# Optimization experiments

Measured on AMD Instinct MI355X. Metric: run time of the kernel, lower is better.

The kernel has to match this reference:

```python
import jax, jax.numpy as jnp
import numpy as np

B, S, DIM = 2, 2048, 2048
NH = 16
D_NOPE, D_ROPE, D_V = 128, 64, 128
D_QK = D_NOPE + D_ROPE  # 192
KV_RANK = 512
RMS_EPS = 1e-6


def setup_inputs() -> dict:
    key = jax.random.key(0)
    ks = jax.random.split(key, 8)
    x = jax.random.normal(ks[0], (B, S, DIM), dtype=jnp.float32)
    # rotary freqs as (cos, sin) pairs: [S, D_ROPE//2, 2]
    pos = jnp.arange(S, dtype=jnp.float32)
    inv_freq = 1.0 / (10000.0 ** (jnp.arange(0, D_ROPE, 2, dtype=jnp.float32) / D_ROPE))
    ang = pos[:, None] * inv_freq[None, :]
    freqs_cis = jnp.stack([jnp.cos(ang), jnp.sin(ang)], axis=-1)
    # causal mask [S, S]
    mask = jnp.where(jnp.arange(S)[None, :] > jnp.arange(S)[:, None], -jnp.inf, 0.0).astype(jnp.float32)
    sd = lambda k, shp, fan: jax.random.normal(k, shp, dtype=jnp.float32) * (fan ** -0.5)
    wq = sd(ks[1], (NH * D_QK, DIM), DIM)
    wkv_a = sd(ks[2], (KV_RANK + D_ROPE, DIM), DIM)
    wkv_b = sd(ks[3], (NH * (D_NOPE + D_V), KV_RANK), KV_RANK)
    wo = sd(ks[4], (DIM, NH * D_V), NH * D_V)
    kv_norm_w = jnp.ones((KV_RANK,), dtype=jnp.float32)
    return {"x": x, "start_pos": 0, "freqs_cis": freqs_cis, "mask": mask,
            "wq": wq, "wkv_a": wkv_a, "wkv_b": wkv_b, "wo": wo, "kv_norm_w": kv_norm_w}


def _rope(x, freqs):
    # x: [b, s, h, d] with d even; freqs: [s, d//2, 2] (cos, sin)
    b, s, h, d = x.shape
    xr = x.reshape(b, s, h, d // 2, 2)
    cos = freqs[None, :, None, :, 0]
    sin = freqs[None, :, None, :, 1]
    ye = xr[..., 0] * cos - xr[..., 1] * sin
    yo = xr[..., 0] * sin + xr[..., 1] * cos
    return jnp.stack([ye, yo], axis=-1).reshape(b, s, h, d)


def _rms_norm(x, w):
    var = jnp.mean(jnp.square(x), axis=-1, keepdims=True)
    return x * jax.lax.rsqrt(var + RMS_EPS) * w


def reference(x, start_pos, freqs_cis, mask, wq, wkv_a, wkv_b, wo, kv_norm_w):
    b, s, _ = x.shape
    scale = D_QK ** -0.5
    # query projection -> [b, s, h, d_qk]
    q = jnp.einsum('bsd,ed->bse', x, wq).reshape(b, s, NH, D_QK)
    q_nope, q_pe = q[..., :D_NOPE], q[..., D_NOPE:]
    q_pe = _rope(q_pe, freqs_cis)
    q = jnp.concatenate([q_nope, q_pe], axis=-1)
    # latent kv projection -> [b, s, kv_rank + d_rope]
    kv = jnp.einsum('bsd,ed->bse', x, wkv_a)
    kv_lat, k_pe = kv[..., :KV_RANK], kv[..., KV_RANK:]
    k_pe = _rope(k_pe[:, :, None, :], freqs_cis)  # [b, s, 1, d_rope]
    kv_up = jnp.einsum('bsr,er->bse', _rms_norm(kv_lat, kv_norm_w), wkv_b)
    kv_up = kv_up.reshape(b, s, NH, D_NOPE + D_V)
    k_nope, v = kv_up[..., :D_NOPE], kv_up[..., D_NOPE:]
    k = jnp.concatenate([k_nope, jnp.broadcast_to(k_pe, (b, s, NH, D_ROPE))], axis=-1)
    # start_pos = 0 prefill: cache[:end_pos] == freshly computed k, v
    scores = jnp.einsum('bshd,bthd->bsht', q, k) * scale
    if mask is not None:
        scores = scores + mask[None, :, None, :]
    probs = jax.nn.softmax(scores.astype(jnp.float32), axis=-1).astype(x.dtype)
    out = jnp.einsum('bsht,bthd->bshd', probs, v)
    return jnp.einsum('bse,de->bsd', out.reshape(b, s, NH * D_V), wo)
```

## Files before the change

### kernel.cpp

```cpp
#include <hip/hip_runtime.h>
#include <hip/hip_bf16.h>


typedef __bf16 bf16x8 __attribute__((ext_vector_type(8)));
typedef float  f32x4  __attribute__((ext_vector_type(4)));
typedef float  f32x16 __attribute__((ext_vector_type(16)));
typedef unsigned short us8 __attribute__((ext_vector_type(8)));
typedef unsigned short us4 __attribute__((ext_vector_type(4)));
typedef unsigned int   ui4 __attribute__((ext_vector_type(4)));

#define S_LEN   2048
#define BS_TOT  4096
#define NH      16
#define DQK     192
#define DV      128
#define KV_RANK 512
#define QSTR    3840

__device__ inline unsigned short f2bf(float f) {
  __hip_bfloat16 h = __float2bfloat16(f);
  return *reinterpret_cast<unsigned short*>(&h);
}
__device__ inline float bfu2f(unsigned short u) {
  unsigned int x = ((unsigned int)u) << 16;
  return __builtin_bit_cast(float, x);
}
__device__ inline unsigned int pack2bf(float a, float b) {
  return (unsigned int)f2bf(a) | ((unsigned int)f2bf(b) << 16);
}
__device__ inline void glds16(const void* g, void* l) {
  __builtin_amdgcn_global_load_lds(
      (const __attribute__((address_space(1))) unsigned int*)g,
      (__attribute__((address_space(3))) unsigned int*)l, 16, 0, 0);
}

__global__ __launch_bounds__(256) void cast_all_kernel(
    const float* __restrict__ x, const float* __restrict__ wq,
    const float* __restrict__ wkva, const float* __restrict__ wkvb,
    const float* __restrict__ wo,
    __hip_bfloat16* __restrict__ xb, __hip_bfloat16* __restrict__ wqb,
    __hip_bfloat16* __restrict__ wkvab, __hip_bfloat16* __restrict__ wkvbb,
    __hip_bfloat16* __restrict__ wob) {
  const int bid = blockIdx.x;
  const float* src; __hip_bfloat16* dst; int n, npad, b0, nb;
  if (bid < 771)       { src = x;    dst = xb;    n = 8388608; npad = 8388608; b0 = 0;    nb = 771; }
  else if (bid < 1349) { src = wq;   dst = wqb;   n = 6291456; npad = 6291456; b0 = 771;  nb = 578; }
  else if (bid < 1469) { src = wkva; dst = wkvab; n = 1179648; npad = 1572864; b0 = 1349; nb = 120; }
  else if (bid < 1662) { src = wkvb; dst = wkvbb; n = 2097152; npad = 2097152; b0 = 1469; nb = 193; }
  else                 { src = wo;   dst = wob;   n = 4194304; npad = 4194304; b0 = 1662; nb = 386; }
  const int tid = (bid - b0) * 256 + threadIdx.x;
  const int stride = nb * 256;
  for (int i = tid * 4; i < npad; i += stride * 4) {
    if (i + 3 < n) {
      f32x4 v = *(const f32x4*)(src + i);
      dst[i + 0] = __float2bfloat16(v.x);
      dst[i + 1] = __float2bfloat16(v.y);
      dst[i + 2] = __float2bfloat16(v.z);
      dst[i + 3] = __float2bfloat16(v.w);
    } else {
#pragma unroll
      for (int z = 0; z < 4; z++)
        dst[i + z] = __float2bfloat16((i + z < n) ? src[i + z] : 0.f);
    }
  }
}

template<int OUT_BF16>
__global__ __launch_bounds__(512, 2) void gemm_bt256(
    const __hip_bfloat16* __restrict__ A, const __hip_bfloat16* __restrict__ Bw,
    void* __restrict__ Cp, int M, int N, int K, int nbx) {
  __shared__ alignas(16) unsigned short Asl[2][256 * 64];
  __shared__ alignas(16) unsigned short Bsl[2][256 * 64];

  const int nwg = gridDim.x;
  const int cpx = nwg >> 3;
  const int id  = (blockIdx.x & 7) * cpx + (blockIdx.x >> 3);
  const int bx = id % nbx, by = id / nbx;
  const int m0 = by * 256, n0 = bx * 256;

  const int tid = threadIdx.x, w = tid >> 6, lane = tid & 63;
  const int wr = w >> 2, wc = w & 3;
  const int ml = lane & 15, quad = lane >> 4;
  const int srow = w * 8 + (lane >> 3);
  const int scol = ((lane & 7) ^ (lane >> 3)) * 8;

  const unsigned short* Ag = (const unsigned short*)A + (size_t)(m0 + srow) * K + scol;
  const unsigned short* Bg = (const unsigned short*)Bw + (size_t)(n0 + srow) * K + scol;

  f32x4 acc[8][4];
#pragma unroll
  for (int i = 0; i < 8; i++)
#pragma unroll
    for (int j = 0; j < 4; j++)
#pragma unroll
      for (int e = 0; e < 4; e++) acc[i][j][e] = 0.0f;

  auto stage = [&](int slot, int k0) {
#pragma unroll
    for (int j = 0; j < 4; j++)
      glds16(Ag + (size_t)j * 64 * K + k0, &Asl[slot][(j * 64 + w * 8) * 64]);
#pragma unroll
    for (int j = 0; j < 4; j++)
      glds16(Bg + (size_t)j * 64 * K + k0, &Bsl[slot][(j * 64 + w * 8) * 64]);
  };

  const int nt = K / 64;
  stage(0, 0);
  stage(1, 64);
  asm volatile("s_waitcnt vmcnt(8)" ::: "memory");
  __builtin_amdgcn_s_barrier();
  asm volatile("" ::: "memory");

  int slot = 0;
  for (int t = 0; t < nt; ++t) {
    const unsigned short* As = &Asl[slot][0];
    const unsigned short* Bs = &Bsl[slot][0];

    bf16x8 bfr[2][2][2];
#pragma unroll
    for (int nh = 0; nh < 2; nh++)
#pragma unroll
      for (int nf = 0; nf < 2; nf++) {
        int r = wc * 64 + nh * 32 + nf * 16 + ml;
        const char* rowp = (const char*)&Bs[r * 64];
#pragma unroll
        for (int ks = 0; ks < 2; ks++)
          bfr[nh][nf][ks] =
              *(const bf16x8*)(rowp + ((ks * 64 + quad * 16) ^ ((ml & 7) << 4)));
      }
#pragma unroll
    for (int mh = 0; mh < 2; mh++) {
      bf16x8 af[4][2];
#pragma unroll
      for (int mf = 0; mf < 4; mf++) {
        int r = wr * 128 + mh * 64 + mf * 16 + ml;
        const char* rowp = (const char*)&As[r * 64];
#pragma unroll
        for (int ks = 0; ks < 2; ks++)
          af[mf][ks] =
              *(const bf16x8*)(rowp + ((ks * 64 + quad * 16) ^ ((ml & 7) << 4)));
      }
      __builtin_amdgcn_s_setprio(1);
#pragma unroll
      for (int nh = 0; nh < 2; nh++)
#pragma unroll
        for (int mf = 0; mf < 4; mf++)
#pragma unroll
          for (int nf = 0; nf < 2; nf++)
#pragma unroll
            for (int ks = 0; ks < 2; ks++)
              acc[mh * 4 + mf][nh * 2 + nf] = __builtin_amdgcn_mfma_f32_16x16x32_bf16(
                  af[mf][ks], bfr[nh][nf][ks], acc[mh * 4 + mf][nh * 2 + nf], 0, 0, 0);
      __builtin_amdgcn_s_setprio(0);
    }

    asm volatile("" ::: "memory");
    __builtin_amdgcn_s_barrier();
    asm volatile("" ::: "memory");
    if (t + 2 < nt) {
      stage(slot, (t + 2) * 64);
      asm volatile("s_waitcnt vmcnt(8)" ::: "memory");
    } else {
      asm volatile("s_waitcnt vmcnt(0)" ::: "memory");
    }
    __builtin_amdgcn_s_barrier();
    asm volatile("" ::: "memory");
    slot ^= 1;
  }

#pragma unroll
  for (int mi = 0; mi < 8; mi++) {
#pragma unroll
    for (int ni = 0; ni < 4; ni++) {
      int col = n0 + wc * 64 + ni * 16 + ml;
      int rowb = m0 + wr * 128 + mi * 16 + quad * 4;
#pragma unroll
      for (int j = 0; j < 4; j++) {
        float v = acc[mi][ni][j];
        if (OUT_BF16)
          ((__hip_bfloat16*)Cp)[(size_t)(rowb + j) * N + col] = __float2bfloat16(v);
        else
          ((float*)Cp)[(size_t)(rowb + j) * N + col] = v;
      }
    }
  }
}

template<int OUT_BF16>
__global__ __launch_bounds__(512, 1) void gemm_bt256x128(
    const __hip_bfloat16* __restrict__ A, const __hip_bfloat16* __restrict__ Bw,
    void* __restrict__ Cp, int M, int N, int K, int nbx) {
  __shared__ alignas(16) unsigned short Asl[2][256 * 64];
  __shared__ alignas(16) unsigned short Bsl[2][128 * 64];

  const int nwg = gridDim.x;
  const int cpx = nwg >> 3;
  const int id  = (blockIdx.x & 7) * cpx + (blockIdx.x >> 3);
  const int bx = id % nbx, by = id / nbx;
  const int m0 = by * 256, n0 = bx * 128;

  const int tid = threadIdx.x, w = tid >> 6, lane = tid & 63;
  const int wr = w >> 2, wc = w & 3;
  const int ml = lane & 15, quad = lane >> 4;
  const int srow = w * 8 + (lane >> 3);
  const int scol = ((lane & 7) ^ (lane >> 3)) * 8;

  const unsigned short* Ag = (const unsigned short*)A + (size_t)(m0 + srow) * K + scol;
  const unsigned short* Bg = (const unsigned short*)Bw + (size_t)(n0 + srow) * K + scol;

  f32x4 acc[8][2];
#pragma unroll
  for (int i = 0; i < 8; i++)
#pragma unroll
    for (int j = 0; j < 2; j++)
#pragma unroll
      for (int e = 0; e < 4; e++) acc[i][j][e] = 0.0f;

  auto stage = [&](int slot, int k0) {
#pragma unroll
    for (int j = 0; j < 4; j++)
      glds16(Ag + (size_t)j * 64 * K + k0, &Asl[slot][(j * 64 + w * 8) * 64]);
#pragma unroll
    for (int j = 0; j < 2; j++)
      glds16(Bg + (size_t)j * 64 * K + k0, &Bsl[slot][(j * 64 + w * 8) * 64]);
  };

  const int nt = K / 64;
  stage(0, 0);
  stage(1, 64);
  asm volatile("s_waitcnt vmcnt(6)" ::: "memory");
  __builtin_amdgcn_s_barrier();
  asm volatile("" ::: "memory");

  int slot = 0;
  for (int t = 0; t < nt; ++t) {
    const unsigned short* As = &Asl[slot][0];
    const unsigned short* Bs = &Bsl[slot][0];

    bf16x8 bfr[2][2];
#pragma unroll
    for (int nf = 0; nf < 2; nf++) {
      int r = wc * 32 + nf * 16 + ml;
      const char* rowp = (const char*)&Bs[r * 64];
#pragma unroll
      for (int ks = 0; ks < 2; ks++)
        bfr[nf][ks] =
            *(const bf16x8*)(rowp + ((ks * 64 + quad * 16) ^ ((ml & 7) << 4)));
    }
#pragma unroll
    for (int mh = 0; mh < 2; mh++) {
      bf16x8 af[4][2];
#pragma unroll
      for (int mf = 0; mf < 4; mf++) {
        int r = wr * 128 + mh * 64 + mf * 16 + ml;
        const char* rowp = (const char*)&As[r * 64];
#pragma unroll
        for (int ks = 0; ks < 2; ks++)
          af[mf][ks] =
              *(const bf16x8*)(rowp + ((ks * 64 + quad * 16) ^ ((ml & 7) << 4)));
      }
      __builtin_amdgcn_s_setprio(1);
#pragma unroll
      for (int mf = 0; mf < 4; mf++)
#pragma unroll
        for (int nf = 0; nf < 2; nf++)
#pragma unroll
          for (int ks = 0; ks < 2; ks++)
            acc[mh * 4 + mf][nf] = __builtin_amdgcn_mfma_f32_16x16x32_bf16(
                af[mf][ks], bfr[nf][ks], acc[mh * 4 + mf][nf], 0, 0, 0);
      __builtin_amdgcn_s_setprio(0);
    }

    asm volatile("" ::: "memory");
    __builtin_amdgcn_s_barrier();
    asm volatile("" ::: "memory");
    if (t + 2 < nt) {
      stage(slot, (t + 2) * 64);
      asm volatile("s_waitcnt vmcnt(6)" ::: "memory");
    } else {
      asm volatile("s_waitcnt vmcnt(0)" ::: "memory");
    }
    __builtin_amdgcn_s_barrier();
    asm volatile("" ::: "memory");
    slot ^= 1;
  }

#pragma unroll
  for (int mi = 0; mi < 8; mi++) {
#pragma unroll
    for (int ni = 0; ni < 2; ni++) {
      int col = n0 + wc * 32 + ni * 16 + ml;
      int rowb = m0 + wr * 128 + mi * 16 + quad * 4;
#pragma unroll
      for (int j = 0; j < 4; j++) {
        float v = acc[mi][ni][j];
        if (OUT_BF16)
          ((__hip_bfloat16*)Cp)[(size_t)(rowb + j) * N + col] = __float2bfloat16(v);
        else
          ((float*)Cp)[(size_t)(rowb + j) * N + col] = v;
      }
    }
  }
}

__global__ __launch_bounds__(256) void rope_rms_kernel(
    __hip_bfloat16* __restrict__ qkv, const float* __restrict__ w,
    const float* __restrict__ freqs, __hip_bfloat16* __restrict__ latent,
    __hip_bfloat16* __restrict__ kpe_out) {
  int si = blockIdx.x;
  int s  = si & (S_LEN - 1);
  int tid = threadIdx.x;
#pragma unroll
  for (int p = tid; p < NH * 32; p += 256) {
    int h = p >> 5, i = p & 31;
    size_t base = (size_t)si * QSTR + h * DQK + 128 + 2 * i;
    float c  = freqs[s * 64 + 2 * i];
    float sn = freqs[s * 64 + 2 * i + 1];
    float x0 = __bfloat162float(qkv[base]);
    float x1 = __bfloat162float(qkv[base + 1]);
    qkv[base]     = __float2bfloat16(x0 * c - x1 * sn);
    qkv[base + 1] = __float2bfloat16(x0 * sn + x1 * c);
  }
  const unsigned short* row = (const unsigned short*)qkv + (size_t)si * QSTR + 3072;
  float v0 = bfu2f(row[tid]), v1 = bfu2f(row[tid + 256]);
  float ss = v0 * v0 + v1 * v1;
#pragma unroll
  for (int off = 1; off < 64; off <<= 1) ss += __shfl_xor(ss, off, 64);
  __shared__ float red[4];
  if ((tid & 63) == 0) red[tid >> 6] = ss;
  __syncthreads();
  float tot = red[0] + red[1] + red[2] + red[3];
  float r = rsqrtf(tot / 512.0f + 1e-6f);
  latent[(size_t)si * 512 + tid]       = __float2bfloat16(v0 * r * w[tid]);
  latent[(size_t)si * 512 + tid + 256] = __float2bfloat16(v1 * r * w[tid + 256]);
  if (tid < 32) {
    float c  = freqs[s * 64 + 2 * tid];
    float sn = freqs[s * 64 + 2 * tid + 1];
    float x0 = bfu2f(row[512 + 2 * tid]), x1 = bfu2f(row[512 + 2 * tid + 1]);
    kpe_out[(size_t)si * 64 + 2 * tid]     = __float2bfloat16(x0 * c - x1 * sn);
    kpe_out[(size_t)si * 64 + 2 * tid + 1] = __float2bfloat16(x0 * sn + x1 * c);
  }
}

__global__ __launch_bounds__(512, 2) void attn_mfma_kernel(
    const __hip_bfloat16* __restrict__ qb,
    const __hip_bfloat16* __restrict__ kvup,
    const __hip_bfloat16* __restrict__ kpe,
    unsigned short* __restrict__ op0,
    unsigned short* __restrict__ op1,
    float* __restrict__ mlp0,
    float* __restrict__ mlp1) {
  constexpr int KS = 200;
  constexpr int VS = 36;
  __shared__ alignas(16) unsigned short Ks[2][64 * KS];
  __shared__ alignas(16) unsigned int   Vt2[2][128 * VS];

  const int id = blockIdx.x;
  const int x  = id >> 5;
  const int hb = id & 31;
  const int h  = hb >> 1, b = hb & 1;

  const int tid = threadIdx.x, wave = tid >> 6, lane = tid & 63;
  const int l31 = lane & 31, hh = lane >> 5;
  const float qs2 = 0.07216878364870322f * 1.4426950408889634f;

  const int m16 = tid & 15;
  const int hp  = tid >> 4;
  const int vkey = (m16 & 7) << 2;
  const unsigned short* kvbase = (const unsigned short*)kvup;
  const unsigned short* kpbase = (const unsigned short*)kpe;

  int kr_[3], kc_[3];
#pragma unroll
  for (int it = 0; it < 3; it++) {
    int slot = tid + it * 512;
    kr_[it] = slot / 24;
    kc_[it] = slot - kr_[it] * 24;
  }

#pragma unroll 1
  for (int item = 0; item < 2; ++item) {
    const int qt2    = item ? (7 - x) : x;
    const int kstart = item ? (2 * qt2 + 2) : 0;
    const int kend   = kstart + 2 * qt2 + 2;
    const int qwb = qt2 * 256 + wave * 32;
    const int qg  = qwb + l31;

    bf16x8 Qf[12];
    {
      const unsigned short* qrow = (const unsigned short*)qb +
          (size_t)(b * S_LEN + qg) * QSTR + h * DQK;
#pragma unroll
      for (int s = 0; s < 12; s++)
        Qf[s] = *(const bf16x8*)(qrow + s * 16 + hh * 8);
    }

    float m_i = -1e30f, l_i = 0.0f;
    f32x16 O2[4];
#pragma unroll
    for (int mt = 0; mt < 4; mt++)
#pragma unroll
      for (int j = 0; j < 16; j++) O2[mt][j] = 0.0f;

    us8 Kpre[3], Vpre[2];

    const unsigned short* kptr[3];
    int kstep[3];
#pragma unroll
    for (int it = 0; it < 3; it++) {
      if (kc_[it] < 16) {
        kptr[it] = kvbase + (size_t)(b * S_LEN + kstart * 64 + kr_[it]) * (NH * 256)
                   + h * 256 + kc_[it] * 8;
        kstep[it] = 64 * NH * 256;
      } else {
        kptr[it] = kpbase + (size_t)(b * S_LEN + kstart * 64 + kr_[it]) * 64
                   + (kc_[it] - 16) * 8;
        kstep[it] = 64 * 64;
      }
    }
    const unsigned short* vptr = kvbase +
        (size_t)(b * S_LEN + kstart * 64 + 2 * hp) * (NH * 256) + h * 256 + 128 + m16 * 8;

    if (item) __syncthreads();

    {
#pragma unroll
      for (int it = 0; it < 3; it++) {
        Kpre[it] = *(const us8*)kptr[it];
        kptr[it] += kstep[it];
      }
      Vpre[0] = *(const us8*)vptr;
      Vpre[1] = *(const us8*)(vptr + NH * 256);
      vptr += 64 * NH * 256;
#pragma unroll
      for (int it = 0; it < 3; it++)
        *(us8*)&Ks[0][kr_[it] * KS + kc_[it] * 8] = Kpre[it];
#pragma unroll
      for (int z = 0; z < 8; z++) {
        int d = m16 * 8 + z;
        Vt2[0][d * VS + (hp ^ vkey)] =
            (unsigned)(unsigned short)Vpre[0][z] |
            ((unsigned)(unsigned short)Vpre[1][z] << 16);
      }
      __syncthreads();
    }

    int cur = 0;
    for (int kt = kstart; kt < kend; kt++) {
      const int kb = kt * 64;
      const unsigned short* ksc = Ks[cur];
      const unsigned int*   vtc = Vt2[cur];

      const int havenext = (kt + 1 < kend);
      if (havenext) {
#pragma unroll
        for (int it = 0; it < 3; it++) {
          Kpre[it] = *(const us8*)kptr[it];
          kptr[it] += kstep[it];
        }
        Vpre[0] = *(const us8*)vptr;
        Vpre[1] = *(const us8*)(vptr + NH * 256);
        vptr += 64 * NH * 256;
      }

      if (kb <= qwb + 31) {
        f32x16 st2[2];
        __builtin_amdgcn_s_setprio(1);
#pragma unroll
        for (int mt = 0; mt < 2; mt++) {
          f32x16 acc;
#pragma unroll
          for (int j = 0; j < 16; j++) acc[j] = 0.0f;
#pragma unroll
          for (int s = 0; s < 12; s++) {
            bf16x8 kf = *(const bf16x8*)&ksc[(mt * 32 + l31) * KS + s * 16 + hh * 8];
            acc = __builtin_amdgcn_mfma_f32_32x32x16_bf16(kf, Qf[s], acc, 0, 0, 0);
          }
          st2[mt] = acc;
        }
        __builtin_amdgcn_s_setprio(0);

        if (kb + 64 > qwb) {
#pragma unroll
          for (int mt = 0; mt < 2; mt++)
#pragma unroll
            for (int r = 0; r < 16; r++) {
              int kpos = kb + mt * 32 + (r & 3) + 8 * (r >> 2) + 4 * hh;
              st2[mt][r] = (kpos > qg) ? -1e30f : st2[mt][r];
            }
        }
        float t16[16];
#pragma unroll
        for (int r = 0; r < 16; r++) t16[r] = fmaxf(st2[0][r], st2[1][r]);
#pragma unroll
        for (int sw = 8; sw >= 1; sw >>= 1)
#pragma unroll
          for (int r = 0; r < 8; r++)
            if (r < sw) t16[r] = fmaxf(t16[r], t16[r + sw]);
        float mloc = t16[0] * qs2;
        mloc = fmaxf(mloc, __shfl_xor(mloc, 32, 64));
        if (!__all(mloc <= m_i + 8.0f)) {
          float m_new = fmaxf(m_i, mloc);
          float alpha = exp2f(m_i - m_new);
          l_i *= alpha;
#pragma unroll
          for (int mt = 0; mt < 4; mt++)
#pragma unroll
            for (int j = 0; j < 16; j++) O2[mt][j] *= alpha;
          m_i = m_new;
        }
        const float nm = -m_i;
#pragma unroll
        for (int mt = 0; mt < 2; mt++)
#pragma unroll
          for (int r = 0; r < 16; r++) {
            float p = exp2f(fmaf(st2[mt][r], qs2, nm));
            st2[mt][r] = p;
          }
        float s16[16];
#pragma unroll
        for (int r = 0; r < 16; r++) s16[r] = st2[0][r] + st2[1][r];
#pragma unroll
        for (int sw = 8; sw >= 1; sw >>= 1)
#pragma unroll
          for (int r = 0; r < 8; r++)
            if (r < sw) s16[r] += s16[r + sw];
        float psum = s16[0];
        psum += __shfl_xor(psum, 32, 64);
        l_i += psum;

        bf16x8 pf[4];
#pragma unroll
        for (int ss = 0; ss < 4; ss++) {
          const int pmt = ss >> 1, gg = ss & 1;
          unsigned int U0 = pack2bf(st2[pmt][gg * 8 + 0], st2[pmt][gg * 8 + 1]);
          unsigned int U1 = pack2bf(st2[pmt][gg * 8 + 2], st2[pmt][gg * 8 + 3]);
          unsigned int U2 = pack2bf(st2[pmt][gg * 8 + 4], st2[pmt][gg * 8 + 5]);
          unsigned int U3 = pack2bf(st2[pmt][gg * 8 + 6], st2[pmt][gg * 8 + 7]);
          unsigned int E0 = __shfl_xor(hh ? U0 : U2, 32, 64);
          unsigned int E1 = __shfl_xor(hh ? U1 : U3, 32, 64);
          ui4 pd;
          pd.x = hh ? E0 : U0;
          pd.y = hh ? E1 : U1;
          pd.z = hh ? U2 : E0;
          pd.w = hh ? U3 : E1;
          pf[ss] = __builtin_bit_cast(bf16x8, pd);
        }

        __builtin_amdgcn_s_setprio(1);
#pragma unroll
        for (int ss = 0; ss < 4; ss++) {
#pragma unroll
          for (int mt = 0; mt < 4; mt++) {
            int v = mt * 32 + l31;
            const unsigned int* vp =
                &vtc[v * VS + ((ss * 8 + hh * 4) ^ (((v >> 3) & 7) << 2))];
            bf16x8 bv = *(const bf16x8*)vp;
            O2[mt] = __builtin_amdgcn_mfma_f32_32x32x16_bf16(bv, pf[ss], O2[mt],
                                                             0, 0, 0);
          }
        }
        __builtin_amdgcn_s_setprio(0);
      }

      if (havenext) {
#pragma unroll
        for (int it = 0; it < 3; it++)
          *(us8*)&Ks[cur ^ 1][kr_[it] * KS + kc_[it] * 8] = Kpre[it];
#pragma unroll
        for (int z = 0; z < 8; z++) {
          int d = m16 * 8 + z;
          Vt2[cur ^ 1][d * VS + (hp ^ vkey)] =
              (unsigned)(unsigned short)Vpre[0][z] |
              ((unsigned)(unsigned short)Vpre[1][z] << 16);
        }
        __syncthreads();
        cur ^= 1;
      }
    }

    unsigned short* op = item ? op1 : op0;
    float* mlp = item ? mlp1 : mlp0;
    const size_t basep = (size_t)(b * S_LEN + qg) * NH + h;
    unsigned short* orow = op + basep * 128;
#pragma unroll
    for (int mt = 0; mt < 4; mt++) {
#pragma unroll
      for (int g = 0; g < 4; g++) {
        us4 pk;
#pragma unroll
        for (int j = 0; j < 4; j++) pk[j] = f2bf(O2[mt][g * 4 + j]);
        *(us4*)(orow + mt * 32 + g * 8 + hh * 4) = pk;
      }
    }
    if (hh == 0) {
      mlp[basep * 2 + 0] = m_i;
      mlp[basep * 2 + 1] = l_i;
    }
  }
}

__global__ __launch_bounds__(256) void attn_combine_kernel(
    const unsigned short* __restrict__ op0, const unsigned short* __restrict__ op1,
    const float* __restrict__ mlp0, const float* __restrict__ mlp1,
    __hip_bfloat16* __restrict__ attn_out) {
  const int bs = blockIdx.x;
  const int tid = threadIdx.x;
  const int h = tid >> 4, dc = (tid & 15) * 8;
  const size_t basep = (size_t)bs * NH + h;
  const us8 a = *(const us8*)(op0 + basep * 128 + dc);
  const us8 c = *(const us8*)(op1 + basep * 128 + dc);
  const float m0 = mlp0[basep * 2], l0 = mlp0[basep * 2 + 1];
  const float m1 = mlp1[basep * 2], l1 = mlp1[basep * 2 + 1];
  const float m = fmaxf(m0, m1);
  const float a0 = exp2f(m0 - m), a1 = exp2f(m1 - m);
  const float inv = 1.0f / (l0 * a0 + l1 * a1);
  us8 o;
#pragma unroll
  for (int z = 0; z < 8; z++) {
    float v = (bfu2f((unsigned short)a[z]) * a0 +
               bfu2f((unsigned short)c[z]) * a1) * inv;
    o[z] = f2bf(v);
  }
  *(us8*)((unsigned short*)attn_out + (size_t)bs * (NH * DV) + h * DV + dc) = o;
}

extern "C" void kernel_launch(void* const* d_in, const int* in_sizes, int n_in,
                              void* d_out, int out_size, void* d_ws, size_t ws_size,
                              hipStream_t stream) {
  const float* x     = (const float*)d_in[0];
  const float* freqs = (const float*)d_in[2];
  const float* wq    = (const float*)d_in[4];
  const float* wkva  = (const float*)d_in[5];
  const float* wkvb  = (const float*)d_in[6];
  const float* wo    = (const float*)d_in[7];
  const float* kvnw  = (const float*)d_in[8];
  float* out = (float*)d_out;

  char* ws = (char*)d_ws;
  size_t off = 0;
  auto alloc = [&](size_t bytes) {
    void* p = ws + off;
    off += (bytes + 255) & ~(size_t)255;
    return p;
  };
  __hip_bfloat16* x_bf    = (__hip_bfloat16*)alloc((size_t)BS_TOT * 2048 * 2);
  __hip_bfloat16* wq_bf   = (__hip_bfloat16*)alloc((size_t)3072 * 2048 * 2);
  __hip_bfloat16* wkva_bf = (__hip_bfloat16*)alloc((size_t)768 * 2048 * 2);
  __hip_bfloat16* wkvb_bf = (__hip_bfloat16*)alloc((size_t)4096 * 512 * 2);
  __hip_bfloat16* wo_bf   = (__hip_bfloat16*)alloc((size_t)2048 * 2048 * 2);
  __hip_bfloat16* qkv_bf  = (__hip_bfloat16*)alloc((size_t)BS_TOT * QSTR * 2);
  __hip_bfloat16* latent  = (__hip_bfloat16*)alloc((size_t)BS_TOT * 512 * 2);
  __hip_bfloat16* kpe     = (__hip_bfloat16*)alloc((size_t)BS_TOT * 64 * 2);
  __hip_bfloat16* kvup    = (__hip_bfloat16*)alloc((size_t)BS_TOT * 4096 * 2);
  __hip_bfloat16* attn    = (__hip_bfloat16*)alloc((size_t)BS_TOT * 2048 * 2);

  unsigned short* op0 = (unsigned short*)x_bf;
  unsigned short* op1 = (unsigned short*)wq_bf;
  float* mlp0 = (float*)latent;
  float* mlp1 = mlp0 + (size_t)BS_TOT * NH * 2;

  cast_all_kernel<<<2048, 256, 0, stream>>>(x, wq, wkva, wkvb, wo,
                                            x_bf, wq_bf, wkva_bf, wkvb_bf, wo_bf);

  gemm_bt256<1><<<dim3(240), 512, 0, stream>>>(
      x_bf, wq_bf, qkv_bf, BS_TOT, QSTR, 2048, QSTR / 256);
  rope_rms_kernel<<<BS_TOT, 256, 0, stream>>>(qkv_bf, kvnw, freqs, latent, kpe);

  gemm_bt256<1><<<dim3(256), 512, 0, stream>>>(
      latent, wkvb_bf, kvup, BS_TOT, 4096, 512, 16);

  attn_mfma_kernel<<<dim3(256, 1, 1), 512, 0, stream>>>(
      qkv_bf, kvup, kpe, op0, op1, mlp0, mlp1);
  attn_combine_kernel<<<dim3(BS_TOT, 1, 1), 256, 0, stream>>>(
      op0, op1, mlp0, mlp1, attn);

  gemm_bt256x128<0><<<dim3(256), 512, 0, stream>>>(
      attn, wo_bf, out, BS_TOT, 2048, 2048, 16);
}
```

Before: 245.8 us.

## Software-pipeline softmax and PV of previous tile behind current QK MFMAs

The exp, row-sum, bf16 packing and P·V MFMAs of each key tile are deferred until after the QK^T MFMAs of the next tile have been issued. The aim is to let the transcendental and VALU softmax work overlap with matrix-core work. The V tile stays live one extra iteration, so V shared memory goes from double to triple buffering. Deferred scores are kept in extra registers. This adds register pressure and LDS footprint, which risks spills or lower occupancy.

```diff
diff --git a/kernel.cpp b/kernel.cpp
--- a/kernel.cpp
+++ b/kernel.cpp
@@ -353,7 +353,7 @@
   constexpr int KS = 200;
   constexpr int VS = 36;
   __shared__ alignas(16) unsigned short Ks[2][64 * KS];
-  __shared__ alignas(16) unsigned int   Vt2[2][128 * VS];
+  __shared__ alignas(16) unsigned int   Vt3[3][128 * VS];
 
   const int id = blockIdx.x;
   const int x  = id >> 5;
@@ -438,18 +438,74 @@
 #pragma unroll
       for (int z = 0; z < 8; z++) {
         int d = m16 * 8 + z;
-        Vt2[0][d * VS + (hp ^ vkey)] =
+        Vt3[0][d * VS + (hp ^ vkey)] =
             (unsigned)(unsigned short)Vpre[0][z] |
             ((unsigned)(unsigned short)Vpre[1][z] << 16);
       }
       __syncthreads();
     }
 
-    int cur = 0;
+    bool have_prev = false;
+    f32x16 sp[2];
+    const unsigned int* vtp = &Vt3[0][0];
+
+    auto finish_prev = [&]() {
+      const float nm = -m_i;
+#pragma unroll
+      for (int mt = 0; mt < 2; mt++)
+#pragma unroll
+        for (int r = 0; r < 16; r++)
+          sp[mt][r] = exp2f(fmaf(sp[mt][r], qs2, nm));
+      float s16[16];
+#pragma unroll
+      for (int r = 0; r < 16; r++) s16[r] = sp[0][r] + sp[1][r];
+#pragma unroll
+      for (int sw = 8; sw >= 1; sw >>= 1)
+#pragma unroll
+        for (int r = 0; r < 8; r++)
+          if (r < sw) s16[r] += s16[r + sw];
+      float psum = s16[0];
+      psum += __shfl_xor(psum, 32, 64);
+      l_i += psum;
+
+      bf16x8 pf[4];
+#pragma unroll
+      for (int ss = 0; ss < 4; ss++) {
+        const int pmt = ss >> 1, gg = ss & 1;
+        unsigned int U0 = pack2bf(sp[pmt][gg * 8 + 0], sp[pmt][gg * 8 + 1]);
+        unsigned int U1 = pack2bf(sp[pmt][gg * 8 + 2], sp[pmt][gg * 8 + 3]);
+        unsigned int U2 = pack2bf(sp[pmt][gg * 8 + 4], sp[pmt][gg * 8 + 5]);
+        unsigned int U3 = pack2bf(sp[pmt][gg * 8 + 6], sp[pmt][gg * 8 + 7]);
+        unsigned int E0 = __shfl_xor(hh ? U0 : U2, 32, 64);
+        unsigned int E1 = __shfl_xor(hh ? U1 : U3, 32, 64);
+        ui4 pd;
+        pd.x = hh ? E0 : U0;
+        pd.y = hh ? E1 : U1;
+        pd.z = hh ? U2 : E0;
+        pd.w = hh ? U3 : E1;
+        pf[ss] = __builtin_bit_cast(bf16x8, pd);
+      }
+      __builtin_amdgcn_s_setprio(1);
+#pragma unroll
+      for (int ss = 0; ss < 4; ss++) {
+#pragma unroll
+        for (int mt = 0; mt < 4; mt++) {
+          int v = mt * 32 + l31;
+          const unsigned int* vp =
+              &vtp[v * VS + ((ss * 8 + hh * 4) ^ (((v >> 3) & 7) << 2))];
+          bf16x8 bv = *(const bf16x8*)vp;
+          O2[mt] = __builtin_amdgcn_mfma_f32_32x32x16_bf16(bv, pf[ss], O2[mt],
+                                                           0, 0, 0);
+        }
+      }
+      __builtin_amdgcn_s_setprio(0);
+    };
+
     for (int kt = kstart; kt < kend; kt++) {
+      const int u  = kt - kstart;
       const int kb = kt * 64;
-      const unsigned short* ksc = Ks[cur];
-      const unsigned int*   vtc = Vt2[cur];
+      const unsigned short* ksc = Ks[u & 1];
+      const unsigned int*   vtc = &Vt3[u % 3][0];
 
       const int havenext = (kt + 1 < kend);
       if (havenext) {
@@ -479,6 +535,8 @@
           st2[mt] = acc;
         }
         __builtin_amdgcn_s_setprio(0);
+
+        if (have_prev) finish_prev();
 
         if (kb + 64 > qwb) {
 #pragma unroll
@@ -509,74 +567,35 @@
             for (int j = 0; j < 16; j++) O2[mt][j] *= alpha;
           m_i = m_new;
         }
-        const float nm = -m_i;
-#pragma unroll
-        for (int mt = 0; mt < 2; mt++)
-#pragma unroll
-          for (int r = 0; r < 16; r++) {
-            float p = exp2f(fmaf(st2[mt][r], qs2, nm));
-            st2[mt][r] = p;
-          }
-        float s16[16];
-#pragma unroll
-        for (int r = 0; r < 16; r++) s16[r] = st2[0][r] + st2[1][r];
-#pragma unroll
-        for (int sw = 8; sw >= 1; sw >>= 1)
-#pragma unroll
-          for (int r = 0; r < 8; r++)
-            if (r < sw) s16[r] += s16[r + sw];
-        float psum = s16[0];
-        psum += __shfl_xor(psum, 32, 64);
-        l_i += psum;
-
-        bf16x8 pf[4];
-#pragma unroll
-        for (int ss = 0; ss < 4; ss++) {
-          const int pmt = ss >> 1, gg = ss & 1;
-          unsigned int U0 = pack2bf(st2[pmt][gg * 8 + 0], st2[pmt][gg * 8 + 1]);
-          unsigned int U1 = pack2bf(st2[pmt][gg * 8 + 2], st2[pmt][gg * 8 + 3]);
-          unsigned int U2 = pack2bf(st2[pmt][gg * 8 + 4], st2[pmt][gg * 8 + 5]);
-          unsigned int U3 = pack2bf(st2[pmt][gg * 8 + 6], st2[pmt][gg * 8 + 7]);
-          unsigned int E0 = __shfl_xor(hh ? U0 : U2, 32, 64);
-          unsigned int E1 = __shfl_xor(hh ? U1 : U3, 32, 64);
-          ui4 pd;
-          pd.x = hh ? E0 : U0;
-          pd.y = hh ? E1 : U1;
-          pd.z = hh ? U2 : E0;
-          pd.w = hh ? U3 : E1;
-          pf[ss] = __builtin_bit_cast(bf16x8, pd);
-        }
-
-        __builtin_amdgcn_s_setprio(1);
-#pragma unroll
-        for (int ss = 0; ss < 4; ss++) {
-#pragma unroll
-          for (int mt = 0; mt < 4; mt++) {
-            int v = mt * 32 + l31;
-            const unsigned int* vp =
-                &vtc[v * VS + ((ss * 8 + hh * 4) ^ (((v >> 3) & 7) << 2))];
-            bf16x8 bv = *(const bf16x8*)vp;
-            O2[mt] = __builtin_amdgcn_mfma_f32_32x32x16_bf16(bv, pf[ss], O2[mt],
-                                                             0, 0, 0);
-          }
-        }
-        __builtin_amdgcn_s_setprio(0);
+
+        sp[0] = st2[0];
+        sp[1] = st2[1];
+        vtp = vtc;
+        have_prev = true;
+      } else if (have_prev) {
+        finish_prev();
+        have_prev = false;
       }
 
       if (havenext) {
 #pragma unroll
         for (int it = 0; it < 3; it++)
-          *(us8*)&Ks[cur ^ 1][kr_[it] * KS + kc_[it] * 8] = Kpre[it];
+          *(us8*)&Ks[(u + 1) & 1][kr_[it] * KS + kc_[it] * 8] = Kpre[it];
+        unsigned int* vtn = &Vt3[(u + 1) % 3][0];
 #pragma unroll
         for (int z = 0; z < 8; z++) {
           int d = m16 * 8 + z;
-          Vt2[cur ^ 1][d * VS + (hp ^ vkey)] =
+          vtn[d * VS + (hp ^ vkey)] =
               (unsigned)(unsigned short)Vpre[0][z] |
               ((unsigned)(unsigned short)Vpre[1][z] << 16);
         }
         __syncthreads();
-        cur ^= 1;
-      }
+      }
+    }
+
+    if (have_prev) {
+      finish_prev();
+      have_prev = false;
     }
 
     unsigned short* op = item ? op1 : op0;
```

Result: slower. 259.9 us (+5.7%).
